# Kernel tuning notes

Measured on AMD Instinct MI355X. Metric: run time of the kernel, lower is better.

## Reference

```python
import jax, jax.numpy as jnp
import numpy as np

N_NODES = 100000


def _gcn_conv(h, src, dst, norm, W, b):
    # h: [N, F_in] -> [N, F_out]; aggregate normalized messages over edges
    h = h @ W                                   # transform first (cheaper messages)
    msg = h[src] * norm[:, None]                # [E_tot, F_out]
    agg = jax.ops.segment_sum(msg, dst, num_segments=N_NODES)
    return agg + b


def setup_inputs() -> dict:
    key = jax.random.key(0)
    k1, k2, k3, k4 = jax.random.split(key, 4)
    x = jax.random.normal(k1, (N_NODES, 256), dtype=jnp.float32)
    edge_index = jax.random.randint(k2, (2, 1600000), 0, N_NODES, dtype=jnp.int64)
    W1 = jax.random.normal(k3, (256, 128), dtype=jnp.float32) * (1.0 / np.sqrt(256))
    b1 = jnp.zeros((128,), dtype=jnp.float32)
    W2 = jax.random.normal(k4, (128, 40), dtype=jnp.float32) * (1.0 / np.sqrt(128))
    b2 = jnp.zeros((40,), dtype=jnp.float32)
    return {"x": x, "edge_index": edge_index, "W1": W1, "b1": b1, "W2": W2, "b2": b2}


def reference(x, edge_index, W1, b1, W2, b2):
    # add self-loops
    loop = jnp.arange(N_NODES, dtype=edge_index.dtype)
    src = jnp.concatenate([edge_index[0], loop])
    dst = jnp.concatenate([edge_index[1], loop])
    # symmetric normalization D^{-1/2} (A+I) D^{-1/2}
    deg = jax.ops.segment_sum(jnp.ones_like(dst, dtype=x.dtype), dst, num_segments=N_NODES)
    dinv = jax.lax.rsqrt(jnp.maximum(deg, 1.0))
    norm = dinv[src] * dinv[dst]                # [E_tot]

    h = _gcn_conv(x, src, dst, norm, W1, b1)
    h = jax.nn.relu(h)                          # dropout p=0 / eval -> identity
    h = _gcn_conv(h, src, dst, norm, W2, b2)
    return jax.nn.log_softmax(h, axis=1)
```

## Files before the change

### kernel.cpp

```cpp
#include <hip/hip_runtime.h>
#include <hip/hip_fp8.h>
#include <math.h>

#define N_NODES 100000
#define N_EDGES 1600000
#define F_IN 256
#define F_H 128
#define F_OUT 40

#define BIN_SHIFT 9
#define BIN_NODES 512
#define NBIN 196
#define CAP 12288
#define CNT_PAD 16
#define PART_CHUNK 8192

typedef __attribute__((ext_vector_type(8))) short bf16x8;
typedef __attribute__((ext_vector_type(4))) float floatx4;
typedef __attribute__((ext_vector_type(2))) float floatx2;
typedef __attribute__((ext_vector_type(2))) unsigned int uintx2;
typedef __attribute__((ext_vector_type(4))) unsigned int uintx4;

__device__ __forceinline__ unsigned short f2bf(float f) {
    unsigned int u = __float_as_uint(f);
    u += 0x7fffu + ((u >> 16) & 1u);
    return (unsigned short)(u >> 16);
}
__device__ __forceinline__ float bf2f(unsigned short s) { return __uint_as_float(((unsigned int)s) << 16); }

#if defined(__has_builtin)
#if __has_builtin(__builtin_amdgcn_cvt_pk_fp8_f32)
#define HAVE_PK_ENC 1
#endif
#if __has_builtin(__builtin_amdgcn_cvt_pk_f32_fp8)
#define HAVE_PK_DEC 1
#endif
#if __has_builtin(__builtin_amdgcn_cvt_f32_fp8)
#define HAVE_SC_DEC 1
#endif
#endif

__device__ __forceinline__ unsigned char f2f8(float f) {
#ifdef HAVE_PK_ENC
    int r = __builtin_amdgcn_cvt_pk_fp8_f32(f, f, 0, false);
    return (unsigned char)(r & 0xff);
#else
    __hip_fp8_e4m3 t(f);
    return (unsigned char)t.__x;
#endif
}
__device__ __forceinline__ float f82f(unsigned char b) {
#ifdef HAVE_SC_DEC
    return __builtin_amdgcn_cvt_f32_fp8((int)b, 0);
#else
    __hip_fp8_e4m3 t; t.__x = (__hip_fp8_storage_t)b;
    return (float)t;
#endif
}
__device__ __forceinline__ floatx2 f8x2tof(unsigned short u) {
#ifdef HAVE_PK_DEC
    return __builtin_amdgcn_cvt_pk_f32_fp8((int)u, false);
#else
    floatx2 r;
    r.x = f82f((unsigned char)(u & 0xff));
    r.y = f82f((unsigned char)(u >> 8));
    return r;
#endif
}

__device__ __forceinline__ void acc16(uintx4 u, float* a) {
#pragma unroll
    for (int d = 0; d < 4; ++d) {
        floatx2 lo = f8x2tof((unsigned short)(u[d] & 0xffffu));
        floatx2 hi = f8x2tof((unsigned short)(u[d] >> 16));
        a[d * 4 + 0] += lo.x; a[d * 4 + 1] += lo.y;
        a[d * 4 + 2] += hi.x; a[d * 4 + 3] += hi.y;
    }
}

__global__ void k_zero(int* p, int n) {
    int i = blockIdx.x * blockDim.x + threadIdx.x;
    if (i < n) p[i] = 0;
}

__global__ __launch_bounds__(256) void k_part(const int* __restrict__ eidx,
                                              int* __restrict__ gcnt,
                                              unsigned int* __restrict__ parts) {
    __shared__ int hist[4][NBIN];
    __shared__ int sbase[NBIN];
    __shared__ int rcnt[NBIN];
    const int tid = threadIdx.x;
    const int wv = tid >> 6;
    for (int i = tid; i < NBIN; i += 256) {
        hist[0][i] = 0; hist[1][i] = 0; hist[2][i] = 0; hist[3][i] = 0; rcnt[i] = 0;
    }
    __syncthreads();
    const int e0 = blockIdx.x * PART_CHUNK;
    const int e1 = min(e0 + PART_CHUNK, N_EDGES);
    for (int e = e0 + tid; e < e1; e += 256) {
        int d = eidx[N_EDGES + e];
        atomicAdd(&hist[wv][d >> BIN_SHIFT], 1);
    }
    __syncthreads();
    for (int b = tid; b < NBIN; b += 256) {
        int tot = hist[0][b] + hist[1][b] + hist[2][b] + hist[3][b];
        int old = atomicAdd(&gcnt[b * CNT_PAD], tot);
        sbase[b] = b * CAP + old;
    }
    __syncthreads();
    for (int e = e0 + tid; e < e1; e += 256) {
        int d = eidx[N_EDGES + e];
        int s = eidx[e];
        int b = d >> BIN_SHIFT;
        int r = atomicAdd(&rcnt[b], 1);
        parts[sbase[b] + r] = ((unsigned int)s << BIN_SHIFT) | (unsigned int)(d & (BIN_NODES - 1));
    }
}

__global__ __launch_bounds__(256) void k_build(const unsigned int* __restrict__ parts,
                                               const int* __restrict__ gcnt,
                                               int* __restrict__ rowptr,
                                               float* __restrict__ dinv,
                                               int* __restrict__ csr_src) {
    __shared__ int deg[4][BIN_NODES];
    __shared__ int cur[BIN_NODES];
    __shared__ int scan[256];
    const int tid = threadIdx.x;
    const int wv = tid >> 6;
    const int g = blockIdx.x;

    scan[tid] = (tid < NBIN) ? gcnt[tid * CNT_PAD] : 0;
    __syncthreads();
    for (int off = 1; off < 256; off <<= 1) {
        int v = 0;
        if (tid >= off) v = scan[tid - off];
        __syncthreads();
        if (tid >= off) scan[tid] += v;
        __syncthreads();
    }
    const int binBase = (g == 0) ? 0 : scan[g - 1];
    const int cntg = scan[g] - binBase;

    for (int i = tid; i < BIN_NODES; i += 256) {
        deg[0][i] = 0; deg[1][i] = 0; deg[2][i] = 0; deg[3][i] = 0;
    }
    __syncthreads();

    const unsigned int* pp = parts + (size_t)g * CAP;
    for (int i = tid; i < cntg; i += 256)
        atomicAdd(&deg[wv][pp[i] & (BIN_NODES - 1)], 1);
    __syncthreads();

    const int n0 = 2 * tid, n1 = 2 * tid + 1;
    const int d0 = deg[0][n0] + deg[1][n0] + deg[2][n0] + deg[3][n0];
    const int d1 = deg[0][n1] + deg[1][n1] + deg[2][n1] + deg[3][n1];
    scan[tid] = d0 + d1;
    __syncthreads();
    for (int off = 1; off < 256; off <<= 1) {
        int v = 0;
        if (tid >= off) v = scan[tid - off];
        __syncthreads();
        if (tid >= off) scan[tid] += v;
        __syncthreads();
    }
    const int pre = (tid == 0) ? 0 : scan[tid - 1];
    const int p0 = binBase + pre;
    const int p1 = p0 + d0;
    const int node0 = g * BIN_NODES + n0;
    if (node0 < N_NODES)     { rowptr[node0]     = p0; dinv[node0]     = rsqrtf((float)d0 + 1.0f); }
    if (node0 + 1 < N_NODES) { rowptr[node0 + 1] = p1; dinv[node0 + 1] = rsqrtf((float)d1 + 1.0f); }
    cur[n0] = p0;
    cur[n1] = p1;
    __syncthreads();

    for (int i = tid; i < cntg; i += 256) {
        unsigned int u = pp[i];
        int pos = atomicAdd(&cur[u & (BIN_NODES - 1)], 1);
        csr_src[pos] = (int)(u >> BIN_SHIFT);
    }
    if (g == NBIN - 1 && tid == 0) rowptr[N_NODES] = N_EDGES;
}

__global__ void k_cvt_w(const float* __restrict__ W1, const float* __restrict__ W2,
                        short* __restrict__ W1t, short* __restrict__ W2t) {
    int b = blockIdx.x, t = threadIdx.x;
    if (b < 128) {
        int idx = b * 256 + t;
        int n = idx >> 8, k = idx & 255;
        W1t[n * 256 + k] = (short)f2bf(W1[k * 128 + n]);
    } else {
        int idx = (b - 128) * 256 + t;
        if (idx < 48 * 128) {
            int n = idx >> 7, k = idx & 127;
            float v = (n < F_OUT) ? W2[k * F_OUT + n] : 0.f;
            W2t[n * 128 + k] = (short)f2bf(v);
        }
    }
}

__global__ __launch_bounds__(256) void k_gemm1_mfma(const float* __restrict__ x,
                                                    const short* __restrict__ W1t,
                                                    const float* __restrict__ dinv,
                                                    unsigned char* __restrict__ h1f8) {
    __shared__ short As[128 * 40];
    __shared__ short Bs[128 * 264];
    __shared__ float Ds[128];
    const int tid = threadIdx.x;
    const int row0 = blockIdx.x * 128;
    const int w = tid >> 6, l = tid & 63;
    const int l15 = l & 15, q = l >> 4;
    const int ar = tid >> 1;
    const int ak = (tid & 1) * 16;

    {
        const int n = tid >> 1;
        const int kh = (tid & 1) * 128;
#pragma unroll
        for (int i = 0; i < 16; ++i)
            *(bf16x8*)&Bs[n * 264 + kh + i * 8] = *(const bf16x8*)&W1t[n * 256 + kh + i * 8];
    }
    if (tid < 128) {
        int r = row0 + tid;
        Ds[tid] = (r < N_NODES) ? dinv[r] : 0.f;
    }

    floatx4 acc[2][8];
#pragma unroll
    for (int a = 0; a < 2; ++a)
#pragma unroll
        for (int nt = 0; nt < 8; ++nt) acc[a][nt] = (floatx4)0.f;

    const bool arow_ok = (row0 + ar) < N_NODES;
    const float* xp = x + (size_t)(row0 + ar) * F_IN;

    for (int k0 = 0; k0 < F_IN; k0 += 32) {
        bf16x8 av0 = (bf16x8)0, av1 = (bf16x8)0;
        if (arow_ok) {
            floatx4 f0 = *(const floatx4*)(xp + k0 + ak);
            floatx4 f1 = *(const floatx4*)(xp + k0 + ak + 4);
            floatx4 f2 = *(const floatx4*)(xp + k0 + ak + 8);
            floatx4 f3 = *(const floatx4*)(xp + k0 + ak + 12);
            av0[0] = (short)f2bf(f0[0]); av0[1] = (short)f2bf(f0[1]);
            av0[2] = (short)f2bf(f0[2]); av0[3] = (short)f2bf(f0[3]);
            av0[4] = (short)f2bf(f1[0]); av0[5] = (short)f2bf(f1[1]);
            av0[6] = (short)f2bf(f1[2]); av0[7] = (short)f2bf(f1[3]);
            av1[0] = (short)f2bf(f2[0]); av1[1] = (short)f2bf(f2[1]);
            av1[2] = (short)f2bf(f2[2]); av1[3] = (short)f2bf(f2[3]);
            av1[4] = (short)f2bf(f3[0]); av1[5] = (short)f2bf(f3[1]);
            av1[6] = (short)f2bf(f3[2]); av1[7] = (short)f2bf(f3[3]);
        }
        __syncthreads();
        *(bf16x8*)&As[ar * 40 + ak]     = av0;
        *(bf16x8*)&As[ar * 40 + ak + 8] = av1;
        __syncthreads();

        bf16x8 af[2], bfr[8];
#pragma unroll
        for (int a = 0; a < 2; ++a)
            af[a] = *(const bf16x8*)&As[((w * 2 + a) * 16 + l15) * 40 + q * 8];
#pragma unroll
        for (int nt = 0; nt < 8; ++nt)
            bfr[nt] = *(const bf16x8*)&Bs[(nt * 16 + l15) * 264 + k0 + q * 8];
#pragma unroll
        for (int a = 0; a < 2; ++a)
#pragma unroll
            for (int nt = 0; nt < 8; ++nt)
                acc[a][nt] = __builtin_amdgcn_mfma_f32_16x16x32_bf16(af[a], bfr[nt], acc[a][nt], 0, 0, 0);
    }
#pragma unroll
    for (int a = 0; a < 2; ++a) {
#pragma unroll
        for (int r = 0; r < 4; ++r) {
            const int rl = (w * 2 + a) * 16 + q * 4 + r;
            const int row = row0 + rl;
            if (row < N_NODES) {
                const float ds = Ds[rl];
                unsigned char* hp = h1f8 + (size_t)row * F_H;
#pragma unroll
                for (int nt = 0; nt < 8; ++nt)
                    hp[nt * 16 + l15] = f2f8(acc[a][nt][r] * ds);
            }
        }
    }
}

__global__ __launch_bounds__(256) void k_spmm1(const int* __restrict__ rowptr,
                                               const int* __restrict__ csr_src,
                                               const uintx4* __restrict__ h1d4,
                                               const float* __restrict__ dinv,
                                               const float* __restrict__ b1,
                                               unsigned short* __restrict__ agg1b) {
    const int slot = threadIdx.x >> 3;
    const int p = threadIdx.x & 7;
    const int bid = blockIdx.x;
    const int k = bid & 7, j = bid >> 3;
    const int nb = (k < 5) ? (k * 391 + j) : (5 * 391 + (k - 5) * 390 + j);
    const int node = nb * 32 + slot;

    const int beg = rowptr[node];
    const int end = rowptr[node + 1];
    const float dv = dinv[node];

    float accA[16], accB[16];
#pragma unroll
    for (int jj = 0; jj < 16; ++jj) { accA[jj] = 0.f; accB[jj] = 0.f; }
    acc16(h1d4[(size_t)node * 8 + p], accA);

    int i = beg;
    for (; i + 3 < end; i += 4) {
        int s0 = csr_src[i], s1 = csr_src[i + 1], s2 = csr_src[i + 2], s3 = csr_src[i + 3];
        uintx4 u0 = h1d4[(size_t)s0 * 8 + p];
        uintx4 u1 = h1d4[(size_t)s1 * 8 + p];
        uintx4 u2 = h1d4[(size_t)s2 * 8 + p];
        uintx4 u3 = h1d4[(size_t)s3 * 8 + p];
        acc16(u0, accA); acc16(u1, accB);
        acc16(u2, accA); acc16(u3, accB);
    }
    for (; i < end; ++i)
        acc16(h1d4[(size_t)csr_src[i] * 8 + p], accA);

    const float* bp = b1 + 16 * p;
    unsigned int ow[8];
#pragma unroll
    for (int jj = 0; jj < 8; ++jj) {
        float v0 = fmaf(accA[2 * jj]     + accB[2 * jj],     dv, bp[2 * jj]);
        float v1 = fmaf(accA[2 * jj + 1] + accB[2 * jj + 1], dv, bp[2 * jj + 1]);
        v0 = v0 > 0.f ? v0 : 0.f;
        v1 = v1 > 0.f ? v1 : 0.f;
        ow[jj] = ((unsigned int)f2bf(v1) << 16) | f2bf(v0);
    }
    uintx4* op = (uintx4*)(agg1b + (size_t)node * F_H) + 2 * p;
    uintx4 o0, o1;
    o0[0] = ow[0]; o0[1] = ow[1]; o0[2] = ow[2]; o0[3] = ow[3];
    o1[0] = ow[4]; o1[1] = ow[5]; o1[2] = ow[6]; o1[3] = ow[7];
    op[0] = o0;
    op[1] = o1;
}

__global__ __launch_bounds__(256) void k_gemm2_mfma(const unsigned short* __restrict__ agg1b,
                                                    const short* __restrict__ W2t,
                                                    const float* __restrict__ dinv,
                                                    unsigned char* __restrict__ h2f8) {
    __shared__ short As[128 * 40];
    __shared__ short Bs[48 * 136];
    __shared__ float Ds[128];
    const int tid = threadIdx.x;
    const int bidr = blockIdx.x;
    const int kx = bidr & 7, jx = bidr >> 3;
    const int cb = (kx < 6) ? (kx * 98 + jx) : (6 * 98 + (kx - 6) * 97 + jx);
    const int row0 = cb * 128;
    const int w = tid >> 6, l = tid & 63;
    const int l15 = l & 15, q = l >> 4;
    const int ar = tid >> 1;
    const int ak = (tid & 1) * 16;

#pragma unroll
    for (int i = 0; i < 3; ++i) {
        int c = tid * 3 + i;
        int n = c >> 4, koff = (c & 15) * 8;
        *(bf16x8*)&Bs[n * 136 + koff] = *(const bf16x8*)&W2t[n * 128 + koff];
    }
    if (tid < 128) {
        int r = row0 + tid;
        Ds[tid] = (r < N_NODES) ? dinv[r] : 0.f;
    }

    floatx4 acc[2][3];
#pragma unroll
    for (int a = 0; a < 2; ++a)
#pragma unroll
        for (int nt = 0; nt < 3; ++nt) acc[a][nt] = (floatx4)0.f;

    const bool arow_ok = (row0 + ar) < N_NODES;
    const unsigned short* ap = agg1b + (size_t)(row0 + ar) * F_H;

    for (int k0 = 0; k0 < F_H; k0 += 32) {
        bf16x8 a0, a1;
        if (arow_ok) {
            a0 = *(const bf16x8*)(ap + k0 + ak);
            a1 = *(const bf16x8*)(ap + k0 + ak + 8);
        } else {
            a0 = (bf16x8)0; a1 = (bf16x8)0;
        }
        *(bf16x8*)&As[ar * 40 + ak]     = a0;
        *(bf16x8*)&As[ar * 40 + ak + 8] = a1;
        __syncthreads();

        bf16x8 af[2], bfr[3];
#pragma unroll
        for (int a = 0; a < 2; ++a)
            af[a] = *(const bf16x8*)&As[((w * 2 + a) * 16 + l15) * 40 + q * 8];
#pragma unroll
        for (int nt = 0; nt < 3; ++nt)
            bfr[nt] = *(const bf16x8*)&Bs[(nt * 16 + l15) * 136 + k0 + q * 8];
#pragma unroll
        for (int a = 0; a < 2; ++a)
#pragma unroll
            for (int nt = 0; nt < 3; ++nt)
                acc[a][nt] = __builtin_amdgcn_mfma_f32_16x16x32_bf16(af[a], bfr[nt], acc[a][nt], 0, 0, 0);
        __syncthreads();
    }
#pragma unroll
    for (int a = 0; a < 2; ++a) {
#pragma unroll
        for (int nt = 0; nt < 3; ++nt) {
            int col = nt * 16 + l15;
#pragma unroll
            for (int r = 0; r < 4; ++r) {
                int rl = (w * 2 + a) * 16 + q * 4 + r;
                int row = row0 + rl;
                if (row < N_NODES && col < F_OUT)
                    h2f8[(size_t)row * F_OUT + col] = f2f8(acc[a][nt][r] * Ds[rl]);
            }
        }
    }
}

__global__ __launch_bounds__(256) void k_spmm2_lsm(const int* __restrict__ rowptr,
                                                   const int* __restrict__ csr_src,
                                                   const unsigned int* __restrict__ h2d,
                                                   const float* __restrict__ dinv,
                                                   const float* __restrict__ b2,
                                                   float* __restrict__ out) {
    const int qid = threadIdx.x >> 4;
    const int p = threadIdx.x & 15;
    int node = blockIdx.x * 16 + qid;
    bool nvalid = node < N_NODES;
    bool valid = nvalid && (p < 10);
    int nd = nvalid ? node : 0;
    int beg = 0, end = 0;
    if (valid) { beg = rowptr[nd]; end = rowptr[nd + 1]; }
    float dv = dinv[nd];

    float A0 = 0.f, A1 = 0.f, A2 = 0.f, A3 = 0.f;
    float B0 = 0.f, B1 = 0.f, B2 = 0.f, B3 = 0.f;
    if (valid) {
        unsigned int su = h2d[(size_t)nd * 10 + p];
        floatx2 t0 = f8x2tof((unsigned short)(su & 0xffffu));
        floatx2 t1 = f8x2tof((unsigned short)(su >> 16));
        A0 = t0.x; A1 = t0.y; A2 = t1.x; A3 = t1.y;
    }
    int i = beg;
    for (; i + 1 < end; i += 2) {
        int s0 = csr_src[i], s1 = csr_src[i + 1];
        unsigned int u0 = h2d[(size_t)s0 * 10 + p];
        unsigned int u1 = h2d[(size_t)s1 * 10 + p];
        floatx2 a01 = f8x2tof((unsigned short)(u0 & 0xffffu));
        floatx2 a23 = f8x2tof((unsigned short)(u0 >> 16));
        floatx2 b01 = f8x2tof((unsigned short)(u1 & 0xffffu));
        floatx2 b23 = f8x2tof((unsigned short)(u1 >> 16));
        A0 += a01.x; A1 += a01.y; A2 += a23.x; A3 += a23.y;
        B0 += b01.x; B1 += b01.y; B2 += b23.x; B3 += b23.y;
    }
    if (i < end) {
        unsigned int u0 = h2d[(size_t)csr_src[i] * 10 + p];
        floatx2 a01 = f8x2tof((unsigned short)(u0 & 0xffffu));
        floatx2 a23 = f8x2tof((unsigned short)(u0 >> 16));
        A0 += a01.x; A1 += a01.y; A2 += a23.x; A3 += a23.y;
    }

    float v0 = -INFINITY, v1 = -INFINITY, v2 = -INFINITY, v3 = -INFINITY;
    if (valid) {
        float4 bb = *(const float4*)&b2[4 * p];
        v0 = fmaf(A0 + B0, dv, bb.x);
        v1 = fmaf(A1 + B1, dv, bb.y);
        v2 = fmaf(A2 + B2, dv, bb.z);
        v3 = fmaf(A3 + B3, dv, bb.w);
    }
    float m = fmaxf(fmaxf(v0, v1), fmaxf(v2, v3));
#pragma unroll
    for (int off = 1; off < 16; off <<= 1) m = fmaxf(m, __shfl_xor(m, off, 16));
    float e = 0.f;
    if (valid) e = expf(v0 - m) + expf(v1 - m) + expf(v2 - m) + expf(v3 - m);
#pragma unroll
    for (int off = 1; off < 16; off <<= 1) e += __shfl_xor(e, off, 16);
    if (valid) {
        float ls = logf(e);
        floatx4 o;
        o[0] = v0 - m - ls; o[1] = v1 - m - ls; o[2] = v2 - m - ls; o[3] = v3 - m - ls;
        __builtin_nontemporal_store(o, (floatx4*)&out[(size_t)node * F_OUT + 4 * p]);
    }
}

extern "C" void kernel_launch(void* const* d_in, const int* in_sizes, int n_in,
                              void* d_out, int out_size, void* d_ws, size_t ws_size,
                              hipStream_t stream) {
    const float* x = (const float*)d_in[0];
    const int* eidx = (const int*)d_in[1];
    const float* W1 = (const float*)d_in[2];
    const float* b1 = (const float*)d_in[3];
    const float* W2 = (const float*)d_in[4];
    const float* b2 = (const float*)d_in[5];
    float* out = (float*)d_out;

    char* ws = (char*)d_ws;
    int*   gcnt      = (int*)  (ws);
    int*   rowptr    = (int*)  (ws + 400512);
    int*   csr_src   = (int*)  (ws + 1200528);
    float* dinv      = (float*)(ws + 7600528);
    short* W1t       = (short*)(ws + 8000528);
    short* W2t       = (short*)(ws + 8066064);
    unsigned char*  h1f8  = (unsigned char*) (ws + 8078352);
    unsigned short* agg1b = (unsigned short*)(ws + 20878352);
    unsigned int*   parts = (unsigned int*)  (ws + 20878352);
    unsigned char*  h2f8  = (unsigned char*) (ws + 46478352);

    k_zero<<<(NBIN * CNT_PAD + 255) / 256, 256, 0, stream>>>(gcnt, NBIN * CNT_PAD);
    k_part<<<(N_EDGES + PART_CHUNK - 1) / PART_CHUNK, 256, 0, stream>>>(eidx, gcnt, parts);
    k_build<<<NBIN, 256, 0, stream>>>(parts, gcnt, rowptr, dinv, csr_src);

    k_cvt_w<<<152, 256, 0, stream>>>(W1, W2, W1t, W2t);

    k_gemm1_mfma<<<(N_NODES + 127) / 128, 256, 0, stream>>>(x, W1t, dinv, h1f8);
    k_spmm1<<<3125, 256, 0, stream>>>(rowptr, csr_src,
                                      (const uintx4*)h1f8, dinv, b1, agg1b);
    k_gemm2_mfma<<<782, 256, 0, stream>>>(agg1b, W2t, dinv, h2f8);
    k_spmm2_lsm<<<(N_NODES + 15) / 16, 256, 0, stream>>>(rowptr, csr_src,
                                                         (const unsigned int*)h2f8, dinv, b2, out);
}
```

Baseline: 335.3 us.

## Fuse layer-1 SpMM with layer-2 GEMM via shared memory; fold zeroing into weight conversion

Layer-1 aggregation (gather, bias, ReLU, bf16 pack) now runs in the same kernel as the layer-2 MFMA GEMM. Each block aggregates 64 nodes, with 4 threads per node each covering 32 features, and stages the bf16 rows in LDS for the GEMM. This removes the agg1b round trip through global memory and one kernel launch. The gcnt zeroing also moves into k_cvt_w, dropping the separate zero kernel. The trade-off is fewer threads per node in the gather, more registers per thread (64 accumulators) and heavier LDS use, which may lower occupancy and memory-level parallelism in the gather.

```diff
diff --git a/kernel.cpp b/kernel.cpp
--- a/kernel.cpp
+++ b/kernel.cpp
@@ -26,7 +26,6 @@
     u += 0x7fffu + ((u >> 16) & 1u);
     return (unsigned short)(u >> 16);
 }
-__device__ __forceinline__ float bf2f(unsigned short s) { return __uint_as_float(((unsigned int)s) << 16); }
 
 #if defined(__has_builtin)
 #if __has_builtin(__builtin_amdgcn_cvt_pk_fp8_f32)
@@ -76,11 +75,6 @@
         a[d * 4 + 0] += lo.x; a[d * 4 + 1] += lo.y;
         a[d * 4 + 2] += hi.x; a[d * 4 + 3] += hi.y;
     }
-}
-
-__global__ void k_zero(int* p, int n) {
-    int i = blockIdx.x * blockDim.x + threadIdx.x;
-    if (i < n) p[i] = 0;
 }
 
 __global__ __launch_bounds__(256) void k_part(const int* __restrict__ eidx,
@@ -182,7 +176,8 @@
 }
 
 __global__ void k_cvt_w(const float* __restrict__ W1, const float* __restrict__ W2,
-                        short* __restrict__ W1t, short* __restrict__ W2t) {
+                        short* __restrict__ W1t, short* __restrict__ W2t,
+                        int* __restrict__ gcnt) {
     int b = blockIdx.x, t = threadIdx.x;
     if (b < 128) {
         int idx = b * 256 + t;
@@ -195,6 +190,8 @@
             float v = (n < F_OUT) ? W2[k * F_OUT + n] : 0.f;
             W2t[n * 128 + k] = (short)f2bf(v);
         }
+        int z = (b - 128) * 256 + t;
+        if (z < NBIN * CNT_PAD) gcnt[z] = 0;
     }
 }
 
@@ -284,75 +281,17 @@
     }
 }
 
-__global__ __launch_bounds__(256) void k_spmm1(const int* __restrict__ rowptr,
-                                               const int* __restrict__ csr_src,
-                                               const uintx4* __restrict__ h1d4,
-                                               const float* __restrict__ dinv,
-                                               const float* __restrict__ b1,
-                                               unsigned short* __restrict__ agg1b) {
-    const int slot = threadIdx.x >> 3;
-    const int p = threadIdx.x & 7;
-    const int bid = blockIdx.x;
-    const int k = bid & 7, j = bid >> 3;
-    const int nb = (k < 5) ? (k * 391 + j) : (5 * 391 + (k - 5) * 390 + j);
-    const int node = nb * 32 + slot;
-
-    const int beg = rowptr[node];
-    const int end = rowptr[node + 1];
-    const float dv = dinv[node];
-
-    float accA[16], accB[16];
-#pragma unroll
-    for (int jj = 0; jj < 16; ++jj) { accA[jj] = 0.f; accB[jj] = 0.f; }
-    acc16(h1d4[(size_t)node * 8 + p], accA);
-
-    int i = beg;
-    for (; i + 3 < end; i += 4) {
-        int s0 = csr_src[i], s1 = csr_src[i + 1], s2 = csr_src[i + 2], s3 = csr_src[i + 3];
-        uintx4 u0 = h1d4[(size_t)s0 * 8 + p];
-        uintx4 u1 = h1d4[(size_t)s1 * 8 + p];
-        uintx4 u2 = h1d4[(size_t)s2 * 8 + p];
-        uintx4 u3 = h1d4[(size_t)s3 * 8 + p];
-        acc16(u0, accA); acc16(u1, accB);
-        acc16(u2, accA); acc16(u3, accB);
-    }
-    for (; i < end; ++i)
-        acc16(h1d4[(size_t)csr_src[i] * 8 + p], accA);
-
-    const float* bp = b1 + 16 * p;
-    unsigned int ow[8];
-#pragma unroll
-    for (int jj = 0; jj < 8; ++jj) {
-        float v0 = fmaf(accA[2 * jj]     + accB[2 * jj],     dv, bp[2 * jj]);
-        float v1 = fmaf(accA[2 * jj + 1] + accB[2 * jj + 1], dv, bp[2 * jj + 1]);
-        v0 = v0 > 0.f ? v0 : 0.f;
-        v1 = v1 > 0.f ? v1 : 0.f;
-        ow[jj] = ((unsigned int)f2bf(v1) << 16) | f2bf(v0);
-    }
-    uintx4* op = (uintx4*)(agg1b + (size_t)node * F_H) + 2 * p;
-    uintx4 o0, o1;
-    o0[0] = ow[0]; o0[1] = ow[1]; o0[2] = ow[2]; o0[3] = ow[3];
-    o1[0] = ow[4]; o1[1] = ow[5]; o1[2] = ow[6]; o1[3] = ow[7];
-    op[0] = o0;
-    op[1] = o1;
-}
-
-__global__ __launch_bounds__(256) void k_gemm2_mfma(const unsigned short* __restrict__ agg1b,
-                                                    const short* __restrict__ W2t,
-                                                    const float* __restrict__ dinv,
-                                                    unsigned char* __restrict__ h2f8) {
-    __shared__ short As[128 * 40];
+__global__ __launch_bounds__(256) void k_spmm1_gemm2(const int* __restrict__ rowptr,
+                                                     const int* __restrict__ csr_src,
+                                                     const uintx4* __restrict__ h1d4,
+                                                     const float* __restrict__ dinv,
+                                                     const float* __restrict__ b1,
+                                                     const short* __restrict__ W2t,
+                                                     unsigned char* __restrict__ h2f8) {
     __shared__ short Bs[48 * 136];
-    __shared__ float Ds[128];
+    __shared__ unsigned int aggs[64 * 66];
+    __shared__ float Ds[64];
     const int tid = threadIdx.x;
-    const int bidr = blockIdx.x;
-    const int kx = bidr & 7, jx = bidr >> 3;
-    const int cb = (kx < 6) ? (kx * 98 + jx) : (6 * 98 + (kx - 6) * 97 + jx);
-    const int row0 = cb * 128;
-    const int w = tid >> 6, l = tid & 63;
-    const int l15 = l & 15, q = l >> 4;
-    const int ar = tid >> 1;
-    const int ak = (tid & 1) * 16;
 
 #pragma unroll
     for (int i = 0; i < 3; ++i) {
@@ -360,58 +299,91 @@
         int n = c >> 4, koff = (c & 15) * 8;
         *(bf16x8*)&Bs[n * 136 + koff] = *(const bf16x8*)&W2t[n * 128 + koff];
     }
-    if (tid < 128) {
-        int r = row0 + tid;
-        Ds[tid] = (r < N_NODES) ? dinv[r] : 0.f;
-    }
-
-    floatx4 acc[2][3];
-#pragma unroll
-    for (int a = 0; a < 2; ++a)
-#pragma unroll
-        for (int nt = 0; nt < 3; ++nt) acc[a][nt] = (floatx4)0.f;
-
-    const bool arow_ok = (row0 + ar) < N_NODES;
-    const unsigned short* ap = agg1b + (size_t)(row0 + ar) * F_H;
-
+
+    const int bid = blockIdx.x;
+    const int kx = bid & 7, jx = bid >> 3;
+    const int nb = (kx < 3) ? (kx * 196 + jx) : (3 * 196 + (kx - 3) * 195 + jx);
+
+    const int slot = tid >> 2;
+    const int p = tid & 2 ? (tid & 3) : (tid & 3);
+    const int pq = tid & 3;
+    const int node = nb * 64 + slot;
+    const bool valid = node < N_NODES;
+    const int nd = valid ? node : 0;
+    const int beg = rowptr[nd];
+    const int end = valid ? rowptr[nd + 1] : beg;
+    const float dv = dinv[nd];
+    if (pq == 0) Ds[slot] = valid ? dv : 0.f;
+
+    float accA[32], accB[32];
+#pragma unroll
+    for (int jj = 0; jj < 32; ++jj) { accA[jj] = 0.f; accB[jj] = 0.f; }
+
+    const size_t rb = (size_t)nd * 8 + pq * 2;
+    {
+        uintx4 u0 = h1d4[rb];
+        uintx4 u1 = h1d4[rb + 1];
+        acc16(u0, accA); acc16(u1, &accA[16]);
+    }
+    int i = beg;
+    for (; i + 1 < end; i += 2) {
+        int s0 = csr_src[i], s1 = csr_src[i + 1];
+        uintx4 u0 = h1d4[(size_t)s0 * 8 + pq * 2];
+        uintx4 u1 = h1d4[(size_t)s0 * 8 + pq * 2 + 1];
+        uintx4 u2 = h1d4[(size_t)s1 * 8 + pq * 2];
+        uintx4 u3 = h1d4[(size_t)s1 * 8 + pq * 2 + 1];
+        acc16(u0, accA); acc16(u1, &accA[16]);
+        acc16(u2, accB); acc16(u3, &accB[16]);
+    }
+    if (i < end) {
+        int s0 = csr_src[i];
+        uintx4 u0 = h1d4[(size_t)s0 * 8 + pq * 2];
+        uintx4 u1 = h1d4[(size_t)s0 * 8 + pq * 2 + 1];
+        acc16(u0, accA); acc16(u1, &accA[16]);
+    }
+
+    {
+        const float* bp = b1 + 32 * pq;
+        unsigned int* arow = &aggs[slot * 66 + pq * 16];
+#pragma unroll
+        for (int jj = 0; jj < 16; ++jj) {
+            float v0 = fmaf(accA[2 * jj]     + accB[2 * jj],     dv, bp[2 * jj]);
+            float v1 = fmaf(accA[2 * jj + 1] + accB[2 * jj + 1], dv, bp[2 * jj + 1]);
+            v0 = v0 > 0.f ? v0 : 0.f;
+            v1 = v1 > 0.f ? v1 : 0.f;
+            arow[jj] = ((unsigned int)f2bf(v1) << 16) | f2bf(v0);
+        }
+    }
+    __syncthreads();
+
+    const int w = tid >> 6, l = tid & 63;
+    const int l15 = l & 15, q = l >> 4;
+    const short* aggsS = (const short*)aggs;
+
+    floatx4 acc2[3];
+#pragma unroll
+    for (int nt = 0; nt < 3; ++nt) acc2[nt] = (floatx4)0.f;
+
+#pragma unroll
     for (int k0 = 0; k0 < F_H; k0 += 32) {
-        bf16x8 a0, a1;
-        if (arow_ok) {
-            a0 = *(const bf16x8*)(ap + k0 + ak);
-            a1 = *(const bf16x8*)(ap + k0 + ak + 8);
-        } else {
-            a0 = (bf16x8)0; a1 = (bf16x8)0;
-        }
-        *(bf16x8*)&As[ar * 40 + ak]     = a0;
-        *(bf16x8*)&As[ar * 40 + ak + 8] = a1;
-        __syncthreads();
-
-        bf16x8 af[2], bfr[3];
-#pragma unroll
-        for (int a = 0; a < 2; ++a)
-            af[a] = *(const bf16x8*)&As[((w * 2 + a) * 16 + l15) * 40 + q * 8];
+        bf16x8 af = *(const bf16x8*)&aggsS[(w * 16 + l15) * 132 + k0 + q * 8];
+        bf16x8 bfr[3];
 #pragma unroll
         for (int nt = 0; nt < 3; ++nt)
             bfr[nt] = *(const bf16x8*)&Bs[(nt * 16 + l15) * 136 + k0 + q * 8];
 #pragma unroll
-        for (int a = 0; a < 2; ++a)
-#pragma unroll
-            for (int nt = 0; nt < 3; ++nt)
-                acc[a][nt] = __builtin_amdgcn_mfma_f32_16x16x32_bf16(af[a], bfr[nt], acc[a][nt], 0, 0, 0);
-        __syncthreads();
-    }
-#pragma unroll
-    for (int a = 0; a < 2; ++a) {
-#pragma unroll
-        for (int nt = 0; nt < 3; ++nt) {
-            int col = nt * 16 + l15;
-#pragma unroll
-            for (int r = 0; r < 4; ++r) {
-                int rl = (w * 2 + a) * 16 + q * 4 + r;
-                int row = row0 + rl;
-                if (row < N_NODES && col < F_OUT)
-                    h2f8[(size_t)row * F_OUT + col] = f2f8(acc[a][nt][r] * Ds[rl]);
-            }
+        for (int nt = 0; nt < 3; ++nt)
+            acc2[nt] = __builtin_amdgcn_mfma_f32_16x16x32_bf16(af, bfr[nt], acc2[nt], 0, 0, 0);
+    }
+#pragma unroll
+    for (int nt = 0; nt < 3; ++nt) {
+        const int col = nt * 16 + l15;
+#pragma unroll
+        for (int r = 0; r < 4; ++r) {
+            const int rl = w * 16 + q * 4 + r;
+            const int row = nb * 64 + rl;
+            if (row < N_NODES && col < F_OUT)
+                h2f8[(size_t)row * F_OUT + col] = f2f8(acc2[nt][r] * Ds[rl]);
         }
     }
 }
@@ -501,20 +473,16 @@
     short* W1t       = (short*)(ws + 8000528);
     short* W2t       = (short*)(ws + 8066064);
     unsigned char*  h1f8  = (unsigned char*) (ws + 8078352);
-    unsigned short* agg1b = (unsigned short*)(ws + 20878352);
     unsigned int*   parts = (unsigned int*)  (ws + 20878352);
     unsigned char*  h2f8  = (unsigned char*) (ws + 46478352);
 
-    k_zero<<<(NBIN * CNT_PAD + 255) / 256, 256, 0, stream>>>(gcnt, NBIN * CNT_PAD);
+    k_cvt_w<<<152, 256, 0, stream>>>(W1, W2, W1t, W2t, gcnt);
     k_part<<<(N_EDGES + PART_CHUNK - 1) / PART_CHUNK, 256, 0, stream>>>(eidx, gcnt, parts);
     k_build<<<NBIN, 256, 0, stream>>>(parts, gcnt, rowptr, dinv, csr_src);
 
-    k_cvt_w<<<152, 256, 0, stream>>>(W1, W2, W1t, W2t);
-
     k_gemm1_mfma<<<(N_NODES + 127) / 128, 256, 0, stream>>>(x, W1t, dinv, h1f8);
-    k_spmm1<<<3125, 256, 0, stream>>>(rowptr, csr_src,
-                                      (const uintx4*)h1f8, dinv, b1, agg1b);
-    k_gemm2_mfma<<<782, 256, 0, stream>>>(agg1b, W2t, dinv, h2f8);
+    k_spmm1_gemm2<<<1563, 256, 0, stream>>>(rowptr, csr_src,
+                                            (const uintx4*)h1f8, dinv, b1, W2t, h2f8);
     k_spmm2_lsm<<<(N_NODES + 15) / 16, 256, 0, stream>>>(rowptr, csr_src,
                                                          (const unsigned int*)h2f8, dinv, b2, out);
 }
```

After: 341.7 us. Within noise of the previous version (+1.9%).

## Sort nodes by degree to balance work in the SpMM kernels

Applied to the files above, without the earlier changes.

Adds a counting sort of nodes by in-degree (a histogram, a scan and a scatter into a permutation array) so that both SpMM kernels process nodes in degree order. Lanes in a wavefront then see similar edge counts, which cuts divergence and tail imbalance. It also folds the counter zeroing into the weight-conversion kernel so k_zero can be dropped. The costs are three extra small launches, an indirect perm load per node, and scattered writes and reads of node rows, which loses the locality the previous interleaved node mapping had.

```diff
diff --git a/kernel.cpp b/kernel.cpp
--- a/kernel.cpp
+++ b/kernel.cpp
@@ -14,6 +14,7 @@
 #define CAP 12288
 #define CNT_PAD 16
 #define PART_CHUNK 8192
+#define DEGB 64
 
 typedef __attribute__((ext_vector_type(8))) short bf16x8;
 typedef __attribute__((ext_vector_type(4))) float floatx4;
@@ -26,7 +27,6 @@
     u += 0x7fffu + ((u >> 16) & 1u);
     return (unsigned short)(u >> 16);
 }
-__device__ __forceinline__ float bf2f(unsigned short s) { return __uint_as_float(((unsigned int)s) << 16); }
 
 #if defined(__has_builtin)
 #if __has_builtin(__builtin_amdgcn_cvt_pk_fp8_f32)
@@ -76,11 +76,6 @@
         a[d * 4 + 0] += lo.x; a[d * 4 + 1] += lo.y;
         a[d * 4 + 2] += hi.x; a[d * 4 + 3] += hi.y;
     }
-}
-
-__global__ void k_zero(int* p, int n) {
-    int i = blockIdx.x * blockDim.x + threadIdx.x;
-    if (i < n) p[i] = 0;
 }
 
 __global__ __launch_bounds__(256) void k_part(const int* __restrict__ eidx,
@@ -181,8 +176,82 @@
     if (g == NBIN - 1 && tid == 0) rowptr[N_NODES] = N_EDGES;
 }
 
+__global__ __launch_bounds__(256) void k_dhist(const int* __restrict__ rowptr,
+                                               int* __restrict__ dcnt) {
+    __shared__ int h[4][DEGB];
+    const int tid = threadIdx.x;
+    const int wv = tid >> 6;
+    if (tid < DEGB) { h[0][tid] = 0; h[1][tid] = 0; h[2][tid] = 0; h[3][tid] = 0; }
+    __syncthreads();
+    const int base = blockIdx.x * 1024;
+#pragma unroll
+    for (int j = 0; j < 4; ++j) {
+        int i = base + j * 256 + tid;
+        if (i < N_NODES) {
+            int d = min(rowptr[i + 1] - rowptr[i], DEGB - 1);
+            atomicAdd(&h[wv][d], 1);
+        }
+    }
+    __syncthreads();
+    if (tid < DEGB) {
+        int tot = h[0][tid] + h[1][tid] + h[2][tid] + h[3][tid];
+        if (tot) atomicAdd(&dcnt[tid * CNT_PAD], tot);
+    }
+}
+
+__global__ void k_dscan(int* dcnt) {
+    if (threadIdx.x == 0) {
+        int run = 0;
+        for (int i = 0; i < DEGB; ++i) {
+            int c = dcnt[i * CNT_PAD];
+            dcnt[i * CNT_PAD] = run;
+            run += c;
+        }
+    }
+}
+
+__global__ __launch_bounds__(256) void k_dscat(const int* __restrict__ rowptr,
+                                               int* __restrict__ dcnt,
+                                               int* __restrict__ perm) {
+    __shared__ int h[4][DEGB];
+    __shared__ int base[DEGB];
+    __shared__ int lr[DEGB];
+    const int tid = threadIdx.x;
+    const int wv = tid >> 6;
+    if (tid < DEGB) {
+        h[0][tid] = 0; h[1][tid] = 0; h[2][tid] = 0; h[3][tid] = 0; lr[tid] = 0;
+    }
+    __syncthreads();
+    const int nb = blockIdx.x * 1024;
+    int dg[4];
+#pragma unroll
+    for (int j = 0; j < 4; ++j) {
+        int i = nb + j * 256 + tid;
+        dg[j] = -1;
+        if (i < N_NODES) {
+            dg[j] = min(rowptr[i + 1] - rowptr[i], DEGB - 1);
+            atomicAdd(&h[wv][dg[j]], 1);
+        }
+    }
+    __syncthreads();
+    if (tid < DEGB) {
+        int tot = h[0][tid] + h[1][tid] + h[2][tid] + h[3][tid];
+        base[tid] = tot ? atomicAdd(&dcnt[tid * CNT_PAD], tot) : 0;
+    }
+    __syncthreads();
+#pragma unroll
+    for (int j = 0; j < 4; ++j) {
+        int i = nb + j * 256 + tid;
+        if (dg[j] >= 0) {
+            int r = atomicAdd(&lr[dg[j]], 1);
+            perm[base[dg[j]] + r] = i;
+        }
+    }
+}
+
 __global__ void k_cvt_w(const float* __restrict__ W1, const float* __restrict__ W2,
-                        short* __restrict__ W1t, short* __restrict__ W2t) {
+                        short* __restrict__ W1t, short* __restrict__ W2t,
+                        int* __restrict__ gcnt, int* __restrict__ dcnt) {
     int b = blockIdx.x, t = threadIdx.x;
     if (b < 128) {
         int idx = b * 256 + t;
@@ -195,6 +264,8 @@
             float v = (n < F_OUT) ? W2[k * F_OUT + n] : 0.f;
             W2t[n * 128 + k] = (short)f2bf(v);
         }
+        if (idx < NBIN * CNT_PAD) gcnt[idx] = 0;
+        if (idx < DEGB * CNT_PAD) dcnt[idx] = 0;
     }
 }
 
@@ -286,16 +357,15 @@
 
 __global__ __launch_bounds__(256) void k_spmm1(const int* __restrict__ rowptr,
                                                const int* __restrict__ csr_src,
+                                               const int* __restrict__ perm,
                                                const uintx4* __restrict__ h1d4,
                                                const float* __restrict__ dinv,
                                                const float* __restrict__ b1,
                                                unsigned short* __restrict__ agg1b) {
     const int slot = threadIdx.x >> 3;
     const int p = threadIdx.x & 7;
-    const int bid = blockIdx.x;
-    const int k = bid & 7, j = bid >> 3;
-    const int nb = (k < 5) ? (k * 391 + j) : (5 * 391 + (k - 5) * 390 + j);
-    const int node = nb * 32 + slot;
+    const int gid = blockIdx.x * 32 + slot;
+    const int node = perm[gid];
 
     const int beg = rowptr[node];
     const int end = rowptr[node + 1];
@@ -418,24 +488,24 @@
 
 __global__ __launch_bounds__(256) void k_spmm2_lsm(const int* __restrict__ rowptr,
                                                    const int* __restrict__ csr_src,
+                                                   const int* __restrict__ perm,
                                                    const unsigned int* __restrict__ h2d,
                                                    const float* __restrict__ dinv,
                                                    const float* __restrict__ b2,
                                                    float* __restrict__ out) {
     const int qid = threadIdx.x >> 4;
     const int p = threadIdx.x & 15;
-    int node = blockIdx.x * 16 + qid;
-    bool nvalid = node < N_NODES;
-    bool valid = nvalid && (p < 10);
-    int nd = nvalid ? node : 0;
+    const int gid = blockIdx.x * 16 + qid;
+    const int node = perm[gid];
+    bool valid = (p < 10);
     int beg = 0, end = 0;
-    if (valid) { beg = rowptr[nd]; end = rowptr[nd + 1]; }
-    float dv = dinv[nd];
+    if (valid) { beg = rowptr[node]; end = rowptr[node + 1]; }
+    float dv = dinv[node];
 
     float A0 = 0.f, A1 = 0.f, A2 = 0.f, A3 = 0.f;
     float B0 = 0.f, B1 = 0.f, B2 = 0.f, B3 = 0.f;
     if (valid) {
-        unsigned int su = h2d[(size_t)nd * 10 + p];
+        unsigned int su = h2d[(size_t)node * 10 + p];
         floatx2 t0 = f8x2tof((unsigned short)(su & 0xffffu));
         floatx2 t1 = f8x2tof((unsigned short)(su >> 16));
         A0 = t0.x; A1 = t0.y; A2 = t1.x; A3 = t1.y;
@@ -495,7 +565,9 @@
 
     char* ws = (char*)d_ws;
     int*   gcnt      = (int*)  (ws);
+    int*   dcnt      = (int*)  (ws + 16384);
     int*   rowptr    = (int*)  (ws + 400512);
+    int*   perm      = (int*)  (ws + 800528);
     int*   csr_src   = (int*)  (ws + 1200528);
     float* dinv      = (float*)(ws + 7600528);
     short* W1t       = (short*)(ws + 8000528);
@@ -505,16 +577,18 @@
     unsigned int*   parts = (unsigned int*)  (ws + 20878352);
     unsigned char*  h2f8  = (unsigned char*) (ws + 46478352);
 
-    k_zero<<<(NBIN * CNT_PAD + 255) / 256, 256, 0, stream>>>(gcnt, NBIN * CNT_PAD);
+    k_cvt_w<<<152, 256, 0, stream>>>(W1, W2, W1t, W2t, gcnt, dcnt);
     k_part<<<(N_EDGES + PART_CHUNK - 1) / PART_CHUNK, 256, 0, stream>>>(eidx, gcnt, parts);
     k_build<<<NBIN, 256, 0, stream>>>(parts, gcnt, rowptr, dinv, csr_src);
 
-    k_cvt_w<<<152, 256, 0, stream>>>(W1, W2, W1t, W2t);
+    k_dhist<<<(N_NODES + 1023) / 1024, 256, 0, stream>>>(rowptr, dcnt);
+    k_dscan<<<1, 64, 0, stream>>>(dcnt);
+    k_dscat<<<(N_NODES + 1023) / 1024, 256, 0, stream>>>(rowptr, dcnt, perm);
 
     k_gemm1_mfma<<<(N_NODES + 127) / 128, 256, 0, stream>>>(x, W1t, dinv, h1f8);
-    k_spmm1<<<3125, 256, 0, stream>>>(rowptr, csr_src,
+    k_spmm1<<<3125, 256, 0, stream>>>(rowptr, csr_src, perm,
                                       (const uintx4*)h1f8, dinv, b1, agg1b);
     k_gemm2_mfma<<<782, 256, 0, stream>>>(agg1b, W2t, dinv, h2f8);
-    k_spmm2_lsm<<<(N_NODES + 15) / 16, 256, 0, stream>>>(rowptr, csr_src,
-                                                         (const unsigned int*)h2f8, dinv, b2, out);
-}
+    k_spmm2_lsm<<<6250, 256, 0, stream>>>(rowptr, csr_src, perm,
+                                          (const unsigned int*)h2f8, dinv, b2, out);
+}
```

After: 351.1 us. 1.05x slower.
